# Kernel tuning notes

Measured on AMD Instinct MI355X. Metric: run time of the kernel, lower is better.

## Reference

```python
import jax, jax.numpy as jnp
import numpy as np

VOCAB = 4096
EMBED = 64
NUM_TOKENS = 16
OBS_DIM = 128
HID = 512


def setup_inputs() -> dict:
    key = jax.random.key(0)
    ks = jax.random.split(key, 10)
    s = lambda fan_in: 1.0 / np.sqrt(fan_in)
    inp = {
        "obs": jax.random.normal(ks[0], (1024, 4, OBS_DIM), dtype=jnp.float32),
        "enc_w1": jax.random.normal(ks[1], (OBS_DIM, HID), dtype=jnp.float32) * s(OBS_DIM),
        "enc_b1": jnp.zeros((HID,), dtype=jnp.float32),
        "enc_w2": jax.random.normal(ks[2], (HID, NUM_TOKENS * EMBED), dtype=jnp.float32) * s(HID),
        "enc_b2": jnp.zeros((NUM_TOKENS * EMBED,), dtype=jnp.float32),
        "dec_w1": jax.random.normal(ks[3], (NUM_TOKENS * EMBED, HID), dtype=jnp.float32) * s(NUM_TOKENS * EMBED),
        "dec_b1": jnp.zeros((HID,), dtype=jnp.float32),
        "dec_w2": jax.random.normal(ks[4], (HID, OBS_DIM), dtype=jnp.float32) * s(HID),
        "dec_b2": jnp.zeros((OBS_DIM,), dtype=jnp.float32),
        # nn.Embedding init: uniform(-1/vocab, 1/vocab)
        "codebook": jax.random.uniform(ks[5], (VOCAB, EMBED), dtype=jnp.float32,
                                        minval=-1.0 / VOCAB, maxval=1.0 / VOCAB),
    }
    return inp


def reference(obs, enc_w1, enc_b1, enc_w2, enc_b2, dec_w1, dec_b1, dec_w2, dec_b2, codebook):
    shape = obs.shape  # (B, N, obs_dim)
    x = obs.reshape(-1, shape[-1])  # (BN, obs_dim)
    # encoder MLP
    h = jax.nn.relu(x @ enc_w1 + enc_b1)
    z = (h @ enc_w2 + enc_b2).reshape(-1, NUM_TOKENS, EMBED)  # (BN, n, e)
    b = z.shape[0]
    zf = z.reshape(-1, EMBED)  # (BN*n, e)
    # ||z||^2 + ||c||^2 - 2 z.c  -> (BN*n, vocab)
    dist = (jnp.sum(zf * zf, axis=1, keepdims=True)
            + jnp.sum(codebook * codebook, axis=1)
            - 2.0 * zf @ codebook.T)
    tokens = jnp.argmin(dist, axis=-1)  # (BN*n,)
    z_q = codebook[tokens].reshape(b, NUM_TOKENS, EMBED)
    # straight-through
    dec_in = z + jax.lax.stop_gradient(z_q - z)
    d = dec_in.reshape(b, NUM_TOKENS * EMBED)
    rec = jax.nn.relu(d @ dec_w1 + dec_b1) @ dec_w2 + dec_b2  # (BN, obs_dim)
    z_out = z.reshape(*shape[:-1], NUM_TOKENS, EMBED)
    zq_out = z_q.reshape(*shape[:-1], NUM_TOKENS, EMBED)
    rec_out = rec.reshape(*shape[:-1], OBS_DIM)
    return z_out, zq_out, rec_out
```

## Files before the change

### kernel.cpp

```cpp
#include <hip/hip_runtime.h>
#include <math.h>

#define VOCAB 4096
#define EMBED 64
#define OBSD  128
#define HIDD  512
#define BNR   4096
#define ZR    65536
#define ZD    1024
#define NCHUNK 4
#define CHSZ  (VOCAB / NCHUNK)
#define TCODES 64
#define NTILES (CHSZ / TCODES)

#define MARGIN_SCALED 8.0e-3f

#define SSTR 136
#define GSTR (8 * SSTR)
#define TYPSZ (4 * GSTR)

#define RB 8

typedef _Float16 half8  __attribute__((ext_vector_type(8)));
typedef _Float16 half4  __attribute__((ext_vector_type(4)));
typedef short    bf16x8 __attribute__((ext_vector_type(8)));
typedef float    f32x4  __attribute__((ext_vector_type(4)));

__device__ __forceinline__ f32x4 mfma_f16(half8 a, half8 b, f32x4 c){
  return __builtin_amdgcn_mfma_f32_16x16x32_f16(a,b,c,0,0,0);
}
__device__ __forceinline__ f32x4 mfma_bf(bf16x8 a, bf16x8 b, f32x4 c){
  return __builtin_amdgcn_mfma_f32_16x16x32_bf16(a,b,c,0,0,0);
}
__device__ __forceinline__ unsigned short f2bf(float f){
  union{float f; unsigned u;} x; x.f=f;
  unsigned u = x.u + 0x7fffu + ((x.u>>16)&1u);
  return (unsigned short)(u>>16);
}
__device__ __forceinline__ float bf2f(unsigned short h){
  union{unsigned u; float f;} x; x.u = ((unsigned)h)<<16; return x.f;
}
__device__ __forceinline__ void split3(float w, unsigned short& b1,
                                       unsigned short& b2, unsigned short& b3){
  b1 = f2bf(w); float r  = w - bf2f(b1);
  b2 = f2bf(r); float r2 = r - bf2f(b2);
  b3 = f2bf(r2);
}
__device__ __forceinline__ bf16x8 ldbf(const unsigned short* p){
  return *(const bf16x8*)(const void*)p;
}

__device__ __forceinline__ void ttile(
    float (*lds)[33], const float* __restrict__ src, int R, int C,
    int ti, int tj, int t, unsigned short* __restrict__ q1,
    unsigned short* __restrict__ q2, unsigned short* __restrict__ q3,
    bool three)
{
  const int r = t >> 5, c = t & 31;
  #pragma unroll
  for (int q = 0; q < 4; ++q)
    lds[r + 8 * q][c] = src[(size_t)(ti * 32 + r + 8 * q) * C + tj * 32 + c];
  __syncthreads();
  #pragma unroll
  for (int q = 0; q < 4; ++q) {
    const int wr = r + 8 * q;
    const float v = lds[c][wr];
    const size_t o = (size_t)(tj * 32 + wr) * R + ti * 32 + c;
    if (three) {
      unsigned short b1, b2, b3;
      split3(v, b1, b2, b3);
      q1[o] = b1; q2[o] = b2; q3[o] = b3;
    } else {
      q1[o] = f2bf(v);
    }
  }
}

__global__ __launch_bounds__(256) void prep_all_kernel(
    const float* __restrict__ cb, _Float16* __restrict__ chi,
    float* __restrict__ bcol, double* __restrict__ bcold,
    float* __restrict__ cbT,
    const float* __restrict__ ew1, unsigned short* __restrict__ w1t1,
    unsigned short* __restrict__ w1t2, unsigned short* __restrict__ w1t3,
    const float* __restrict__ ew2, unsigned short* __restrict__ w2t1,
    unsigned short* __restrict__ w2t2, unsigned short* __restrict__ w2t3,
    const float* __restrict__ obs, unsigned short* __restrict__ o1,
    unsigned short* __restrict__ o2, unsigned short* __restrict__ o3,
    const float* __restrict__ dw1, unsigned short* __restrict__ d1t,
    const float* __restrict__ dw2, unsigned short* __restrict__ d2t,
    int* __restrict__ rcnt)
{
  __shared__ float tl[32][33];
  const int b = blockIdx.x;
  const int t = threadIdx.x;
  if (b == 0 && t == 0) *rcnt = 0;
  if (b < 16) {
    int j = b * 256 + t;
    double s = 0.0;
    #pragma unroll 8
    for (int d = 0; d < EMBED; ++d) {
      float c = cb[j * EMBED + d];
      s += (double)c * (double)c;
      chi[j * EMBED + d] = (_Float16)(c * 4096.0f);
      cbT[(size_t)d * VOCAB + j] = c;
    }
    double bd = -0.5 * s * 4096.0;
    bcold[j] = bd;
    bcol[j] = (float)bd;
  } else if (b < 2064) {
    int e = (b - 16) * 256 + t;
    split3(obs[e], o1[e], o2[e], o3[e]);
  } else if (b < 2128) {
    int tt = b - 2064;
    ttile(tl, ew1, OBSD, HIDD, tt >> 4, tt & 15, t, w1t1, w1t2, w1t3, true);
  } else if (b < 2640) {
    int tt = b - 2128;
    ttile(tl, ew2, HIDD, ZD, tt >> 5, tt & 31, t, w2t1, w2t2, w2t3, true);
  } else if (b < 3152) {
    int tt = b - 2640;
    ttile(tl, dw1, ZD, HIDD, tt >> 4, tt & 15, t, d1t, nullptr, nullptr, false);
  } else {
    int tt = b - 3152;
    ttile(tl, dw2, HIDD, OBSD, tt >> 2, tt & 3, t, d2t, nullptr, nullptr, false);
  }
}

template<int NSPLIT, int MS, bool RELU, int OUT>
__global__ __launch_bounds__(512) void gemm_lds_kernel(
    const unsigned short* __restrict__ A1, const unsigned short* __restrict__ A2,
    const unsigned short* __restrict__ A3,
    const unsigned short* __restrict__ B1, const unsigned short* __restrict__ B2,
    const unsigned short* __restrict__ B3,
    const float* __restrict__ bias, int M, int N, int K,
    unsigned short* __restrict__ H1, unsigned short* __restrict__ H2,
    unsigned short* __restrict__ H3,
    float* __restrict__ Z, _Float16* __restrict__ Zhi)
{
  constexpr int BM  = MS * 32;
  constexpr int ASZ = BM * 40;
  constexpr int BSZ = 128 * 40;
  constexpr int ACH = BM * 4;
  constexpr int TCH = ACH + 512;
  __shared__ unsigned short lds[NSPLIT * (ASZ + BSZ)];

  const int tid  = threadIdx.x;
  const int wave = tid >> 6;
  const int lane = tid & 63;
  const int l15  = lane & 15;
  const int lg   = lane >> 4;
  const int wm   = wave >> 2;
  const int wn   = wave & 3;
  const int m0   = blockIdx.x * BM;
  const int n0   = blockIdx.y * 128;

  const unsigned short* Aps[3] = {A1, A2, A3};
  const unsigned short* Bps[3] = {B1, B2, B3};

  size_t goff[2]; int lb[2], pst[2]; bool valid[2], isA[2];
  #pragma unroll
  for (int sl = 0; sl < 2; ++sl) {
    int c = tid + sl * 512;
    valid[sl] = c < TCH;
    bool a = c < ACH;
    isA[sl] = a;
    int cr = a ? c : (c - ACH);
    if (!valid[sl]) cr = 0;
    int row = cr >> 2, o16 = cr & 3;
    goff[sl] = (size_t)(a ? m0 + row : n0 + row) * K + o16 * 8;
    lb[sl]   = (a ? 0 : NSPLIT * ASZ) + row * 40 + o16 * 8;
    pst[sl]  = a ? ASZ : BSZ;
  }

  #pragma unroll
  for (int sl = 0; sl < 2; ++sl) if (valid[sl]) {
    #pragma unroll
    for (int p = 0; p < NSPLIT; ++p)
      *(bf16x8*)(void*)&lds[lb[sl] + p * pst[sl]] =
          ldbf((isA[sl] ? Aps[p] : Bps[p]) + goff[sl]);
  }
  __syncthreads();

  f32x4 accf[MS][2];
  #pragma unroll
  for (int ms = 0; ms < MS; ++ms)
    #pragma unroll
    for (int ns = 0; ns < 2; ++ns)
      accf[ms][ns] = (f32x4){0.f, 0.f, 0.f, 0.f};

  const int KS = K / 32;
  for (int step = 0; step < KS; ++step) {
    bf16x8 nv[NSPLIT][2];
    const bool pre = (step + 1 < KS);
    if (pre) {
      #pragma unroll
      for (int sl = 0; sl < 2; ++sl) if (valid[sl]) {
        #pragma unroll
        for (int p = 0; p < NSPLIT; ++p)
          nv[p][sl] = ldbf((isA[sl] ? Aps[p] : Bps[p]) + goff[sl]
                           + (size_t)(step + 1) * 32);
      }
    }

    bf16x8 af[NSPLIT][MS], bfr[NSPLIT][2];
    #pragma unroll
    for (int ms = 0; ms < MS; ++ms) {
      const int ar = (wm * MS * 16 + ms * 16 + l15) * 40 + lg * 8;
      #pragma unroll
      for (int p = 0; p < NSPLIT; ++p)
        af[p][ms] = *(const bf16x8*)(const void*)&lds[p * ASZ + ar];
    }
    #pragma unroll
    for (int ns = 0; ns < 2; ++ns) {
      const int br = (wn * 32 + ns * 16 + l15) * 40 + lg * 8;
      #pragma unroll
      for (int p = 0; p < NSPLIT; ++p)
        bfr[p][ns] = *(const bf16x8*)(const void*)&lds[NSPLIT * ASZ + p * BSZ + br];
    }

    #pragma unroll
    for (int ms = 0; ms < MS; ++ms)
      #pragma unroll
      for (int ns = 0; ns < 2; ++ns) {
        if constexpr (NSPLIT == 3) {
          f32x4 acc = accf[ms][ns];
          acc = mfma_bf(af[0][ms], bfr[2][ns], acc);
          acc = mfma_bf(af[1][ms], bfr[1][ns], acc);
          acc = mfma_bf(af[2][ms], bfr[0][ns], acc);
          acc = mfma_bf(af[0][ms], bfr[1][ns], acc);
          acc = mfma_bf(af[1][ms], bfr[0][ns], acc);
          acc = mfma_bf(af[0][ms], bfr[0][ns], acc);
          accf[ms][ns] = acc;
        } else {
          accf[ms][ns] = mfma_bf(af[0][ms], bfr[0][ns], accf[ms][ns]);
        }
      }

    __syncthreads();
    if (pre) {
      #pragma unroll
      for (int sl = 0; sl < 2; ++sl) if (valid[sl]) {
        #pragma unroll
        for (int p = 0; p < NSPLIT; ++p)
          *(bf16x8*)(void*)&lds[lb[sl] + p * pst[sl]] = nv[p][sl];
      }
    }
    __syncthreads();
  }

  #pragma unroll
  for (int ms = 0; ms < MS; ++ms)
    #pragma unroll
    for (int ns = 0; ns < 2; ++ns)
      #pragma unroll
      for (int r = 0; r < 4; ++r) {
        int row = m0 + wm * MS * 16 + ms * 16 + lg * 4 + r;
        int col = n0 + wn * 32 + ns * 16 + l15;
        float v = accf[ms][ns][r] + bias[col];
        if constexpr (RELU) v = v > 0.f ? v : 0.f;
        size_t o = (size_t)row * N + col;
        if constexpr (OUT == 0) {
          split3(v, H1[o], H2[o], H3[o]);
        } else if constexpr (OUT == 1) {
          Z[o] = v;
          Zhi[o] = (_Float16)v;
        } else {
          H1[o] = f2bf(v);
        }
      }
}

template<bool RELU, bool OUTBF>
__global__ __launch_bounds__(256) void dec_mfma_kernel(
    const unsigned short* __restrict__ A, const unsigned short* __restrict__ B,
    const float* __restrict__ bias, int M, int N, int K,
    unsigned short* __restrict__ Obf, float* __restrict__ Of)
{
  const int tid  = threadIdx.x;
  const int wave = tid >> 6;
  const int lane = tid & 63;
  const int l15  = lane & 15;
  const int lg   = lane >> 4;
  const int m0 = blockIdx.x * 64 + (wave >> 1) * 32;
  const int n0 = blockIdx.y * 64 + (wave & 1) * 32;

  f32x4 acc[2][2] = {};
  for (int k0 = 0; k0 < K; k0 += 32) {
    bf16x8 a[2], b[2];
    #pragma unroll
    for (int ms = 0; ms < 2; ++ms)
      a[ms] = ldbf(A + (size_t)(m0 + ms * 16 + l15) * K + k0 + lg * 8);
    #pragma unroll
    for (int ns = 0; ns < 2; ++ns)
      b[ns] = ldbf(B + (size_t)(n0 + ns * 16 + l15) * K + k0 + lg * 8);
    #pragma unroll
    for (int ms = 0; ms < 2; ++ms)
      #pragma unroll
      for (int ns = 0; ns < 2; ++ns)
        acc[ms][ns] = mfma_bf(a[ms], b[ns], acc[ms][ns]);
  }
  #pragma unroll
  for (int ms = 0; ms < 2; ++ms)
    #pragma unroll
    for (int ns = 0; ns < 2; ++ns)
      #pragma unroll
      for (int r = 0; r < 4; ++r) {
        int row = m0 + ms * 16 + lg * 4 + r;
        int col = n0 + ns * 16 + l15;
        float v = acc[ms][ns][r] + bias[col];
        if constexpr (RELU) v = v > 0.f ? v : 0.f;
        if constexpr (OUTBF) Obf[(size_t)row * N + col] = f2bf(v);
        else                 Of[(size_t)row * N + col] = v;
      }
}

__global__ __launch_bounds__(1024) void dist_kernel(
    const _Float16* __restrict__ zhi, const _Float16* __restrict__ chi,
    const float* __restrict__ bcol,
    float2* __restrict__ pb2, int* __restrict__ pidx)
{
  __shared__ _Float16 sh[2][TYPSZ];
  __shared__ float    sbc[CHSZ];

  const int tid  = threadIdx.x;
  const int wave = tid >> 6;
  const int lane = tid & 63;
  const int l15  = lane & 15;
  const int lg   = lane >> 4;
  const int rowW = blockIdx.x * 512 + wave * 32;
  const int ch   = blockIdx.y;

  half8 ah0[2], ah1[2];
  #pragma unroll
  for (int s = 0; s < 2; ++s) {
    const size_t base = (size_t)(rowW + s * 16 + l15) * EMBED + lg * 8;
    ah0[s] = *(const half8*)(zhi + base);
    ah1[s] = *(const half8*)(zhi + base + 32);
  }

  const _Float16* gsrc = chi + (size_t)ch * CHSZ * EMBED;
  const int code = tid >> 4, rem = tid & 15, sl = rem >> 1, hf = rem & 1;
  const int ld = (code >> 4) * GSTR + sl * SSTR + (code & 15) * 8 + hf * 4;
  const size_t goff = (size_t)code * EMBED + sl * 8 + hf * 4;

  sbc[tid] = bcol[ch * CHSZ + tid];

  *(half4*)(&sh[0][ld]) = *(const half4*)(gsrc + goff);
  __syncthreads();

  float best[2][4], second[2][4];
  int   bidx[2][4];
  #pragma unroll
  for (int s = 0; s < 2; ++s)
    #pragma unroll
    for (int r = 0; r < 4; ++r) {
      best[s][r] = -INFINITY; second[s][r] = -INFINITY; bidx[s][r] = 0;
    }

  for (int tile = 0; tile < NTILES; ++tile) {
    const int buf = tile & 1;
    half4 v0 = {};
    if (tile + 1 < NTILES)
      v0 = *(const half4*)(gsrc + (size_t)(tile + 1) * (TCODES * EMBED) + goff);

    const _Float16* ph = &sh[buf][0];
    #pragma unroll
    for (int grp = 0; grp < 4; ++grp) {
      const int rb = grp * GSTR + l15 * 8;
      half8 bh0 = *(const half8*)(ph + rb + lg * SSTR);
      half8 bh1 = *(const half8*)(ph + rb + (4 + lg) * SSTR);
      const int cloc = tile * TCODES + grp * 16 + l15;
      const int col  = ch * CHSZ + cloc;
      const float vb = sbc[cloc];
      const f32x4 seed = {vb, vb, vb, vb};
      #pragma unroll
      for (int s = 0; s < 2; ++s) {
        f32x4 acc = seed;
        acc = mfma_f16(ah0[s], bh0, acc);
        acc = mfma_f16(ah1[s], bh1, acc);
        #pragma unroll
        for (int r = 0; r < 4; ++r) {
          float v = acc[r];
          float sn = __builtin_amdgcn_fmed3f(second[s][r], best[s][r], v);
          bool gt = v > best[s][r];
          best[s][r] = gt ? v : best[s][r];
          bidx[s][r] = gt ? col : bidx[s][r];
          second[s][r] = sn;
        }
      }
    }
    if (tile + 1 < NTILES)
      *(half4*)(&sh[buf ^ 1][ld]) = v0;
    __syncthreads();
  }

  #pragma unroll
  for (int m = 1; m <= 8; m <<= 1) {
    #pragma unroll
    for (int s = 0; s < 2; ++s)
      #pragma unroll
      for (int r = 0; r < 4; ++r) {
        float ob = __shfl_xor(best[s][r], m, 64);
        float os = __shfl_xor(second[s][r], m, 64);
        int   oi = __shfl_xor(bidx[s][r], m, 64);
        float mn = fminf(best[s][r], ob);
        second[s][r] = fmaxf(mn, fmaxf(second[s][r], os));
        if (ob > best[s][r]) { best[s][r] = ob; bidx[s][r] = oi; }
      }
  }

  if (l15 == 0) {
    #pragma unroll
    for (int s = 0; s < 2; ++s)
      #pragma unroll
      for (int r = 0; r < 4; ++r) {
        int row = rowW + s * 16 + lg * 4 + r;
        pb2 [(size_t)ch * ZR + row] = make_float2(best[s][r], second[s][r]);
        pidx[(size_t)ch * ZR + row] = bidx[s][r];
      }
  }
}

__global__ __launch_bounds__(256) void merge_kernel(
    const float2* __restrict__ pb2, const int* __restrict__ pidx,
    int* __restrict__ tokens, int* __restrict__ rcnt, int* __restrict__ rrows)
{
  int r = blockIdx.x * 256 + threadIdx.x;
  float b = -INFINITY, s = -INFINITY;
  int bi = 0;
  #pragma unroll
  for (int c = 0; c < NCHUNK; ++c) {
    float2 p = pb2[(size_t)c * ZR + r];
    int    i = pidx[(size_t)c * ZR + r];
    if (p.x > b) { s = fmaxf(b, p.y); b = p.x; bi = i; }
    else         { s = fmaxf(s, p.x); }
  }
  tokens[r] = bi;
  if (b - s < MARGIN_SCALED) {
    int p = atomicAdd(rcnt, 1);
    if (p < ZR) rrows[p] = r;
  }
}

__global__ __launch_bounds__(512) void rescue_kernel(
    const int* __restrict__ cnt, const int* __restrict__ rows,
    const float* __restrict__ z, const float* __restrict__ cbT,
    const double* __restrict__ bcold, int* __restrict__ tokens)
{
  __shared__ double zl[RB][EMBED];
  __shared__ int    ridx[RB];
  __shared__ double swv[8][RB];
  __shared__ int    swi[8][RB];

  int n = *cnt; if (n > ZR) n = ZR;
  int nb = (n + RB - 1) / RB;
  const int tid = threadIdx.x;

  for (int batch = blockIdx.x; batch < nb; batch += gridDim.x) {
    __syncthreads();
    if (tid < RB) {
      int e = batch * RB + tid;
      ridx[tid] = (e < n) ? rows[e] : -1;
    }
    __syncthreads();
    {
      int r = tid >> 6, k = tid & 63;
      int rr = ridx[r];
      zl[r][k] = (rr >= 0) ? (double)z[(size_t)rr * EMBED + k] : 0.0;
    }
    __syncthreads();

    double best[RB]; int bidx[RB];
    #pragma unroll
    for (int r = 0; r < RB; ++r) { best[r] = -1.0e300; bidx[r] = 0; }

    for (int c = 0; c < VOCAB / 512; ++c) {
      const int j = c * 512 + tid;
      double acc[RB] = {};
      #pragma unroll 16
      for (int k = 0; k < EMBED; ++k) {
        double cd = (double)cbT[(size_t)k * VOCAB + j];
        #pragma unroll
        for (int r = 0; r < RB; ++r)
          acc[r] = fma(cd, zl[r][k], acc[r]);
      }
      const double bc = bcold[j];
      #pragma unroll
      for (int r = 0; r < RB; ++r) {
        double s = 4096.0 * acc[r] + bc;
        if (s > best[r]) { best[r] = s; bidx[r] = j; }
      }
    }

    #pragma unroll
    for (int m = 1; m < 64; m <<= 1) {
      #pragma unroll
      for (int r = 0; r < RB; ++r) {
        double ov = __shfl_xor(best[r], m, 64);
        int    oi = __shfl_xor(bidx[r], m, 64);
        if (ov > best[r] || (ov == best[r] && oi < bidx[r])) {
          best[r] = ov; bidx[r] = oi;
        }
      }
    }
    const int wv = tid >> 6, ln = tid & 63;
    if (ln == 0)
      #pragma unroll
      for (int r = 0; r < RB; ++r) { swv[wv][r] = best[r]; swi[wv][r] = bidx[r]; }
    __syncthreads();
    if (tid < RB) {
      int r = tid;
      double bv = swv[0][r]; int bi = swi[0][r];
      #pragma unroll
      for (int w2 = 1; w2 < 8; ++w2) {
        double ov = swv[w2][r]; int oi = swi[w2][r];
        if (ov > bv || (ov == bv && oi < bi)) { bv = ov; bi = oi; }
      }
      if (ridx[r] >= 0) tokens[ridx[r]] = bi;
    }
  }
}

__global__ __launch_bounds__(256) void gather_kernel(
    const int* __restrict__ tokens, const float* __restrict__ cb,
    float* __restrict__ zq, unsigned short* __restrict__ zqb)
{
  int g = blockIdx.x * 256 + threadIdx.x;
  int row = g >> 4;
  int part = g & 15;
  int tok = tokens[row];
  float4 cv = ((const float4*)cb)[tok * 16 + part];
  ((float4*)zq)[g] = cv;
  ushort4 o;
  o.x = f2bf(cv.x); o.y = f2bf(cv.y); o.z = f2bf(cv.z); o.w = f2bf(cv.w);
  ((ushort4*)zqb)[g] = o;
}

extern "C" void kernel_launch(void* const* d_in, const int* in_sizes, int n_in,
                              void* d_out, int out_size, void* d_ws, size_t ws_size,
                              hipStream_t stream)
{
  const float* obs = (const float*)d_in[0];
  const float* ew1 = (const float*)d_in[1];
  const float* eb1 = (const float*)d_in[2];
  const float* ew2 = (const float*)d_in[3];
  const float* eb2 = (const float*)d_in[4];
  const float* dw1 = (const float*)d_in[5];
  const float* db1 = (const float*)d_in[6];
  const float* dw2 = (const float*)d_in[7];
  const float* db2 = (const float*)d_in[8];
  const float* cb  = (const float*)d_in[9];

  float* out_z   = (float*)d_out;
  float* out_zq  = out_z + (size_t)ZR * EMBED;
  float* out_rec = out_z + 2 * (size_t)ZR * EMBED;

  unsigned short* h1 = (unsigned short*)out_zq;
  unsigned short* h2 = h1 + (size_t)BNR * HIDD;
  unsigned short* h3 = h2 + (size_t)BNR * HIDD;

  char* w = (char*)d_ws;
  _Float16* chi  = (_Float16*)w; w += (size_t)VOCAB * EMBED * 2;
  float*    bcol = (float*)w;    w += 64 * 1024;
  double*   bcold = (double*)w;  w += 64 * 1024;
  float*    cbT  = (float*)w;    w += (size_t)VOCAB * EMBED * 4;
  _Float16* zhi  = (_Float16*)w; w += (size_t)ZR * EMBED * 2;
  char*     spare = w;           w += (size_t)ZR * EMBED * 2;
  unsigned short* w1t1 = (unsigned short*)w; w += (size_t)HIDD * OBSD * 2;
  unsigned short* w1t2 = (unsigned short*)w; w += (size_t)HIDD * OBSD * 2;
  unsigned short* w1t3 = (unsigned short*)w; w += (size_t)HIDD * OBSD * 2;
  unsigned short* w2t1 = (unsigned short*)w; w += (size_t)ZD * HIDD * 2;
  unsigned short* w2t2 = (unsigned short*)w; w += (size_t)ZD * HIDD * 2;
  unsigned short* w2t3 = (unsigned short*)w; w += (size_t)ZD * HIDD * 2;
  unsigned short* d1t  = (unsigned short*)w; w += (size_t)HIDD * ZD * 2;
  unsigned short* d2t  = (unsigned short*)w; w += (size_t)OBSD * HIDD * 2;
  int* tokens = (int*)w;  w += (size_t)ZR * 4;
  int* rrows  = (int*)w;  w += (size_t)ZR * 4;
  int* rcnt   = (int*)w;  w += 64;
  float2* pb2 = (float2*)w; w += (size_t)NCHUNK * ZR * 8;
  int*   pidx = (int*)w;    w += (size_t)NCHUNK * ZR * 4;

  unsigned short* o1 = (unsigned short*)zhi;
  unsigned short* o2 = o1 + (size_t)BNR * OBSD;
  unsigned short* o3 = o2 + (size_t)BNR * OBSD;
  unsigned short* zqb  = (unsigned short*)zhi;
  unsigned short* hdec = (unsigned short*)spare;

  prep_all_kernel<<<3216, 256, 0, stream>>>(
      cb, chi, bcol, bcold, cbT,
      ew1, w1t1, w1t2, w1t3,
      ew2, w2t1, w2t2, w2t3,
      obs, o1, o2, o3,
      dw1, d1t, dw2, d2t, rcnt);

  gemm_lds_kernel<3, 1, true, 0><<<dim3(BNR / 32, HIDD / 128), 512, 0, stream>>>(
      o1, o2, o3, w1t1, w1t2, w1t3, eb1, BNR, HIDD, OBSD,
      h1, h2, h3, nullptr, nullptr);
  gemm_lds_kernel<3, 2, false, 1><<<dim3(BNR / 64, ZD / 128), 512, 0, stream>>>(
      h1, h2, h3, w2t1, w2t2, w2t3, eb2, BNR, ZD, HIDD,
      nullptr, nullptr, nullptr, out_z, zhi);

  dist_kernel<<<dim3(ZR / 512, NCHUNK), 1024, 0, stream>>>(
      zhi, chi, bcol, pb2, pidx);
  merge_kernel<<<ZR / 256, 256, 0, stream>>>(pb2, pidx, tokens, rcnt, rrows);
  rescue_kernel<<<512, 512, 0, stream>>>(rcnt, rrows, out_z, cbT, bcold, tokens);
  gather_kernel<<<(ZR * 16) / 256, 256, 0, stream>>>(tokens, cb, out_zq, zqb);

  gemm_lds_kernel<1, 1, true, 2><<<dim3(BNR / 32, HIDD / 128), 512, 0, stream>>>(
      zqb, zqb, zqb, d1t, d1t, d1t, db1, BNR, HIDD, ZD,
      hdec, nullptr, nullptr, nullptr, nullptr);
  dec_mfma_kernel<false, false><<<dim3(BNR / 64, OBSD / 64), 256, 0, stream>>>(
      hdec, d2t, db2, BNR, OBSD, HIDD, nullptr, out_rec);
}
```

Before: 203.4 us.

## Fuse codebook gather into merge/rescue, reuse LDS GEMM for decoder output, prioritize MFMA

Fuses the codebook gather into the merge kernel, which now writes z_q and its bf16 copy directly from a shared token buffer. The rescue kernel rewrites those rows with its exact result, so the tokens array and the separate gather launch go away. The final decoder GEMM now uses the LDS-tiled gemm kernel with a new fp32 output mode instead of the simple direct-load MFMA kernel. The dist kernel also preloads all B fragments before the MFMA loop and raises wave priority with s_setprio around the compute. The fused path relies on rescue running after merge so its overwrites win, and the final GEMM grid now has only 128 blocks.

```diff
diff --git a/kernel.cpp b/kernel.cpp
--- a/kernel.cpp
+++ b/kernel.cpp
@@ -263,53 +263,11 @@
         } else if constexpr (OUT == 1) {
           Z[o] = v;
           Zhi[o] = (_Float16)v;
+        } else if constexpr (OUT == 2) {
+          H1[o] = f2bf(v);
         } else {
-          H1[o] = f2bf(v);
+          Z[o] = v;
         }
-      }
-}
-
-template<bool RELU, bool OUTBF>
-__global__ __launch_bounds__(256) void dec_mfma_kernel(
-    const unsigned short* __restrict__ A, const unsigned short* __restrict__ B,
-    const float* __restrict__ bias, int M, int N, int K,
-    unsigned short* __restrict__ Obf, float* __restrict__ Of)
-{
-  const int tid  = threadIdx.x;
-  const int wave = tid >> 6;
-  const int lane = tid & 63;
-  const int l15  = lane & 15;
-  const int lg   = lane >> 4;
-  const int m0 = blockIdx.x * 64 + (wave >> 1) * 32;
-  const int n0 = blockIdx.y * 64 + (wave & 1) * 32;
-
-  f32x4 acc[2][2] = {};
-  for (int k0 = 0; k0 < K; k0 += 32) {
-    bf16x8 a[2], b[2];
-    #pragma unroll
-    for (int ms = 0; ms < 2; ++ms)
-      a[ms] = ldbf(A + (size_t)(m0 + ms * 16 + l15) * K + k0 + lg * 8);
-    #pragma unroll
-    for (int ns = 0; ns < 2; ++ns)
-      b[ns] = ldbf(B + (size_t)(n0 + ns * 16 + l15) * K + k0 + lg * 8);
-    #pragma unroll
-    for (int ms = 0; ms < 2; ++ms)
-      #pragma unroll
-      for (int ns = 0; ns < 2; ++ns)
-        acc[ms][ns] = mfma_bf(a[ms], b[ns], acc[ms][ns]);
-  }
-  #pragma unroll
-  for (int ms = 0; ms < 2; ++ms)
-    #pragma unroll
-    for (int ns = 0; ns < 2; ++ns)
-      #pragma unroll
-      for (int r = 0; r < 4; ++r) {
-        int row = m0 + ms * 16 + lg * 4 + r;
-        int col = n0 + ns * 16 + l15;
-        float v = acc[ms][ns][r] + bias[col];
-        if constexpr (RELU) v = v > 0.f ? v : 0.f;
-        if constexpr (OUTBF) Obf[(size_t)row * N + col] = f2bf(v);
-        else                 Of[(size_t)row * N + col] = v;
       }
 }
 
@@ -363,20 +321,26 @@
       v0 = *(const half4*)(gsrc + (size_t)(tile + 1) * (TCODES * EMBED) + goff);
 
     const _Float16* ph = &sh[buf][0];
+    half8 bh[4][2];
+    float vbs[4];
     #pragma unroll
     for (int grp = 0; grp < 4; ++grp) {
       const int rb = grp * GSTR + l15 * 8;
-      half8 bh0 = *(const half8*)(ph + rb + lg * SSTR);
-      half8 bh1 = *(const half8*)(ph + rb + (4 + lg) * SSTR);
-      const int cloc = tile * TCODES + grp * 16 + l15;
-      const int col  = ch * CHSZ + cloc;
-      const float vb = sbc[cloc];
+      bh[grp][0] = *(const half8*)(ph + rb + lg * SSTR);
+      bh[grp][1] = *(const half8*)(ph + rb + (4 + lg) * SSTR);
+      vbs[grp] = sbc[tile * TCODES + grp * 16 + l15];
+    }
+    __builtin_amdgcn_s_setprio(1);
+    #pragma unroll
+    for (int grp = 0; grp < 4; ++grp) {
+      const int col = ch * CHSZ + tile * TCODES + grp * 16 + l15;
+      const float vb = vbs[grp];
       const f32x4 seed = {vb, vb, vb, vb};
       #pragma unroll
       for (int s = 0; s < 2; ++s) {
         f32x4 acc = seed;
-        acc = mfma_f16(ah0[s], bh0, acc);
-        acc = mfma_f16(ah1[s], bh1, acc);
+        acc = mfma_f16(ah0[s], bh[grp][0], acc);
+        acc = mfma_f16(ah1[s], bh[grp][1], acc);
         #pragma unroll
         for (int r = 0; r < 4; ++r) {
           float v = acc[r];
@@ -388,6 +352,7 @@
         }
       }
     }
+    __builtin_amdgcn_s_setprio(0);
     if (tile + 1 < NTILES)
       *(half4*)(&sh[buf ^ 1][ld]) = v0;
     __syncthreads();
@@ -422,9 +387,13 @@
 
 __global__ __launch_bounds__(256) void merge_kernel(
     const float2* __restrict__ pb2, const int* __restrict__ pidx,
-    int* __restrict__ tokens, int* __restrict__ rcnt, int* __restrict__ rrows)
-{
-  int r = blockIdx.x * 256 + threadIdx.x;
+    const float* __restrict__ cb, float* __restrict__ zq,
+    unsigned short* __restrict__ zqb,
+    int* __restrict__ rcnt, int* __restrict__ rrows)
+{
+  __shared__ int stok[256];
+  const int base = blockIdx.x * 256;
+  const int r = base + threadIdx.x;
   float b = -INFINITY, s = -INFINITY;
   int bi = 0;
   #pragma unroll
@@ -434,22 +403,38 @@
     if (p.x > b) { s = fmaxf(b, p.y); b = p.x; bi = i; }
     else         { s = fmaxf(s, p.x); }
   }
-  tokens[r] = bi;
+  stok[threadIdx.x] = bi;
   if (b - s < MARGIN_SCALED) {
     int p = atomicAdd(rcnt, 1);
     if (p < ZR) rrows[p] = r;
   }
+  __syncthreads();
+  const int part = threadIdx.x & 15;
+  const int rl0  = threadIdx.x >> 4;
+  #pragma unroll
+  for (int i = 0; i < 16; ++i) {
+    const int rl = rl0 + i * 16;
+    const int tok = stok[rl];
+    float4 cv = ((const float4*)cb)[tok * 16 + part];
+    const int g = (base + rl) * 16 + part;
+    ((float4*)zq)[g] = cv;
+    ushort4 o;
+    o.x = f2bf(cv.x); o.y = f2bf(cv.y); o.z = f2bf(cv.z); o.w = f2bf(cv.w);
+    ((ushort4*)zqb)[g] = o;
+  }
 }
 
 __global__ __launch_bounds__(512) void rescue_kernel(
     const int* __restrict__ cnt, const int* __restrict__ rows,
     const float* __restrict__ z, const float* __restrict__ cbT,
-    const double* __restrict__ bcold, int* __restrict__ tokens)
+    const double* __restrict__ bcold, const float* __restrict__ cb,
+    float* __restrict__ zq, unsigned short* __restrict__ zqb)
 {
   __shared__ double zl[RB][EMBED];
   __shared__ int    ridx[RB];
   __shared__ double swv[8][RB];
   __shared__ int    swi[8][RB];
+  __shared__ int    sfin[RB];
 
   int n = *cnt; if (n > ZR) n = ZR;
   int nb = (n + RB - 1) / RB;
@@ -515,24 +500,20 @@
         double ov = swv[w2][r]; int oi = swi[w2][r];
         if (ov > bv || (ov == bv && oi < bi)) { bv = ov; bi = oi; }
       }
-      if (ridx[r] >= 0) tokens[ridx[r]] = bi;
-    }
-  }
-}
-
-__global__ __launch_bounds__(256) void gather_kernel(
-    const int* __restrict__ tokens, const float* __restrict__ cb,
-    float* __restrict__ zq, unsigned short* __restrict__ zqb)
-{
-  int g = blockIdx.x * 256 + threadIdx.x;
-  int row = g >> 4;
-  int part = g & 15;
-  int tok = tokens[row];
-  float4 cv = ((const float4*)cb)[tok * 16 + part];
-  ((float4*)zq)[g] = cv;
-  ushort4 o;
-  o.x = f2bf(cv.x); o.y = f2bf(cv.y); o.z = f2bf(cv.z); o.w = f2bf(cv.w);
-  ((ushort4*)zqb)[g] = o;
+      sfin[r] = (ridx[r] >= 0) ? bi : -1;
+    }
+    __syncthreads();
+    {
+      int r = tid >> 6, k = tid & 63;
+      int fb = sfin[r];
+      if (fb >= 0) {
+        int rr = ridx[r];
+        float v = cb[(size_t)fb * EMBED + k];
+        zq[(size_t)rr * EMBED + k] = v;
+        zqb[(size_t)rr * EMBED + k] = f2bf(v);
+      }
+    }
+  }
 }
 
 extern "C" void kernel_launch(void* const* d_in, const int* in_sizes, int n_in,
@@ -573,7 +554,6 @@
   unsigned short* w2t3 = (unsigned short*)w; w += (size_t)ZD * HIDD * 2;
   unsigned short* d1t  = (unsigned short*)w; w += (size_t)HIDD * ZD * 2;
   unsigned short* d2t  = (unsigned short*)w; w += (size_t)OBSD * HIDD * 2;
-  int* tokens = (int*)w;  w += (size_t)ZR * 4;
   int* rrows  = (int*)w;  w += (size_t)ZR * 4;
   int* rcnt   = (int*)w;  w += 64;
   float2* pb2 = (float2*)w; w += (size_t)NCHUNK * ZR * 8;
@@ -601,13 +581,15 @@
 
   dist_kernel<<<dim3(ZR / 512, NCHUNK), 1024, 0, stream>>>(
       zhi, chi, bcol, pb2, pidx);
-  merge_kernel<<<ZR / 256, 256, 0, stream>>>(pb2, pidx, tokens, rcnt, rrows);
-  rescue_kernel<<<512, 512, 0, stream>>>(rcnt, rrows, out_z, cbT, bcold, tokens);
-  gather_kernel<<<(ZR * 16) / 256, 256, 0, stream>>>(tokens, cb, out_zq, zqb);
+  merge_kernel<<<ZR / 256, 256, 0, stream>>>(
+      pb2, pidx, cb, out_zq, zqb, rcnt, rrows);
+  rescue_kernel<<<512, 512, 0, stream>>>(
+      rcnt, rrows, out_z, cbT, bcold, cb, out_zq, zqb);
 
   gemm_lds_kernel<1, 1, true, 2><<<dim3(BNR / 32, HIDD / 128), 512, 0, stream>>>(
       zqb, zqb, zqb, d1t, d1t, d1t, db1, BNR, HIDD, ZD,
       hdec, nullptr, nullptr, nullptr, nullptr);
-  dec_mfma_kernel<false, false><<<dim3(BNR / 64, OBSD / 64), 256, 0, stream>>>(
-      hdec, d2t, db2, BNR, OBSD, HIDD, nullptr, out_rec);
-}
+  gemm_lds_kernel<1, 1, false, 3><<<dim3(BNR / 32, OBSD / 128), 512, 0, stream>>>(
+      hdec, hdec, hdec, d2t, d2t, d2t, db2, BNR, OBSD, HIDD,
+      nullptr, nullptr, nullptr, out_rec, nullptr);
+}
```

Measured after the change: 293.1 us. 44.1% more time.

## Rescue one row per block with 16 codes per thread instead of batched rows

Applied to the files above, without the earlier changes.

Restructures the fp64 rescue kernel so each 256-thread block handles a single ambiguous row, with each thread scoring 16 codebook entries, and launches 2048 blocks instead of 512 blocks that each batched 8 rows. The aim is to spread the rescue work across more blocks and cut per-thread double-precision register pressure. The trade-off is that codebook loads are no longer shared across 8 rows, so the transposed codebook is read once per row rather than once per batch of 8, which raises memory traffic when many rows need rescue.

```diff
diff --git a/kernel.cpp b/kernel.cpp
--- a/kernel.cpp
+++ b/kernel.cpp
@@ -18,8 +18,6 @@
 #define SSTR 136
 #define GSTR (8 * SSTR)
 #define TYPSZ (4 * GSTR)
-
-#define RB 8
 
 typedef _Float16 half8  __attribute__((ext_vector_type(8)));
 typedef _Float16 half4  __attribute__((ext_vector_type(4)));
@@ -441,81 +439,61 @@
   }
 }
 
-__global__ __launch_bounds__(512) void rescue_kernel(
+__global__ __launch_bounds__(256) void rescue_kernel(
     const int* __restrict__ cnt, const int* __restrict__ rows,
     const float* __restrict__ z, const float* __restrict__ cbT,
     const double* __restrict__ bcold, int* __restrict__ tokens)
 {
-  __shared__ double zl[RB][EMBED];
-  __shared__ int    ridx[RB];
-  __shared__ double swv[8][RB];
-  __shared__ int    swi[8][RB];
+  __shared__ float  zrow[EMBED];
+  __shared__ double swv[4];
+  __shared__ int    swi[4];
+  __shared__ int    srow;
 
   int n = *cnt; if (n > ZR) n = ZR;
-  int nb = (n + RB - 1) / RB;
-  const int tid = threadIdx.x;
-
-  for (int batch = blockIdx.x; batch < nb; batch += gridDim.x) {
-    __syncthreads();
-    if (tid < RB) {
-      int e = batch * RB + tid;
-      ridx[tid] = (e < n) ? rows[e] : -1;
-    }
-    __syncthreads();
-    {
-      int r = tid >> 6, k = tid & 63;
-      int rr = ridx[r];
-      zl[r][k] = (rr >= 0) ? (double)z[(size_t)rr * EMBED + k] : 0.0;
-    }
-    __syncthreads();
-
-    double best[RB]; int bidx[RB];
-    #pragma unroll
-    for (int r = 0; r < RB; ++r) { best[r] = -1.0e300; bidx[r] = 0; }
-
-    for (int c = 0; c < VOCAB / 512; ++c) {
-      const int j = c * 512 + tid;
-      double acc[RB] = {};
-      #pragma unroll 16
-      for (int k = 0; k < EMBED; ++k) {
-        double cd = (double)cbT[(size_t)k * VOCAB + j];
-        #pragma unroll
-        for (int r = 0; r < RB; ++r)
-          acc[r] = fma(cd, zl[r][k], acc[r]);
-      }
-      const double bc = bcold[j];
-      #pragma unroll
-      for (int r = 0; r < RB; ++r) {
-        double s = 4096.0 * acc[r] + bc;
-        if (s > best[r]) { best[r] = s; bidx[r] = j; }
-      }
-    }
-
+  const int tid  = threadIdx.x;
+  const int wv   = tid >> 6;
+  const int lane = tid & 63;
+
+  for (int e = blockIdx.x; e < n; e += gridDim.x) {
+    __syncthreads();
+    if (tid == 0) srow = rows[e];
+    __syncthreads();
+    const int row = srow;
+    if (tid < EMBED) zrow[tid] = z[(size_t)row * EMBED + tid];
+    __syncthreads();
+
+    double acc[16] = {};
+    for (int k = 0; k < EMBED; ++k) {
+      const double zk = (double)zrow[k];
+      const float* cp = cbT + (size_t)k * VOCAB + tid;
+      #pragma unroll
+      for (int i = 0; i < 16; ++i)
+        acc[i] = fma((double)cp[i * 256], zk, acc[i]);
+    }
+
+    double best = -1.0e300; int bidx = VOCAB;
+    #pragma unroll
+    for (int i = 0; i < 16; ++i) {
+      const int j = i * 256 + tid;
+      double s = 4096.0 * acc[i] + bcold[j];
+      if (s > best) { best = s; bidx = j; }
+    }
     #pragma unroll
     for (int m = 1; m < 64; m <<= 1) {
-      #pragma unroll
-      for (int r = 0; r < RB; ++r) {
-        double ov = __shfl_xor(best[r], m, 64);
-        int    oi = __shfl_xor(bidx[r], m, 64);
-        if (ov > best[r] || (ov == best[r] && oi < bidx[r])) {
-          best[r] = ov; bidx[r] = oi;
-        }
-      }
-    }
-    const int wv = tid >> 6, ln = tid & 63;
-    if (ln == 0)
-      #pragma unroll
-      for (int r = 0; r < RB; ++r) { swv[wv][r] = best[r]; swi[wv][r] = bidx[r]; }
-    __syncthreads();
-    if (tid < RB) {
-      int r = tid;
-      double bv = swv[0][r]; int bi = swi[0][r];
-      #pragma unroll
-      for (int w2 = 1; w2 < 8; ++w2) {
-        double ov = swv[w2][r]; int oi = swi[w2][r];
+      double ov = __shfl_xor(best, m, 64);
+      int    oi = __shfl_xor(bidx, m, 64);
+      if (ov > best || (ov == best && oi < bidx)) { best = ov; bidx = oi; }
+    }
+    if (lane == 0) { swv[wv] = best; swi[wv] = bidx; }
+    __syncthreads();
+    if (tid == 0) {
+      double bv = swv[0]; int bi = swi[0];
+      #pragma unroll
+      for (int w2 = 1; w2 < 4; ++w2) {
+        double ov = swv[w2]; int oi = swi[w2];
         if (ov > bv || (ov == bv && oi < bi)) { bv = ov; bi = oi; }
       }
-      if (ridx[r] >= 0) tokens[ridx[r]] = bi;
+      tokens[row] = bi;
     }
   }
 }
@@ -602,7 +580,8 @@
   dist_kernel<<<dim3(ZR / 512, NCHUNK), 1024, 0, stream>>>(
       zhi, chi, bcol, pb2, pidx);
   merge_kernel<<<ZR / 256, 256, 0, stream>>>(pb2, pidx, tokens, rcnt, rrows);
-  rescue_kernel<<<512, 512, 0, stream>>>(rcnt, rrows, out_z, cbT, bcold, tokens);
+  rescue_kernel<<<2048, 256, 0, stream>>>(
+      rcnt, rrows, out_z, cbT, bcold, tokens);
   gather_kernel<<<(ZR * 16) / 256, 256, 0, stream>>>(tokens, cb, out_zq, zqb);
 
   gemm_lds_kernel<1, 1, true, 2><<<dim3(BNR / 32, HIDD / 128), 512, 0, stream>>>(
```

Result: slower. 406.1 us (+99.7%).
